# Kernel tuning notes

Hardware: AMD Instinct MI355X
Metric: run time of the kernel (lower is better)

The kernel has to match this reference:

```python
import jax, jax.numpy as jnp
import numpy as np

B, T, H, W_SP, C_IN = 8, 16, 64, 64, 32
F = 64  # output_channels


def _conv(x, w):
    # x: (B,H,W,Cin), w: (kh,kw,Cin,Cout), 'same' padding, stride 1
    return jax.lax.conv_general_dilated(
        x, w, window_strides=(1, 1), padding='SAME',
        dimension_numbers=('NHWC', 'HWIO', 'NHWC'))


def setup_inputs() -> dict:
    key = jax.random.key(0)
    k1, k2, k3 = jax.random.split(key, 3)
    x = jax.random.normal(k1, (B, T, H, W_SP, C_IN), dtype=jnp.float32)
    # Keras ConvLSTM2D kernels: gates stacked [i, f, c, o] along last axis
    W = jax.random.normal(k2, (3, 3, C_IN, 4 * F), dtype=jnp.float32) * 0.05
    U = jax.random.normal(k3, (3, 3, F, 4 * F), dtype=jnp.float32) * 0.05
    b = jnp.zeros((4 * F,), dtype=jnp.float32)
    return {"x": x, "W": W, "U": U, "b": b}


def reference(x, W, U, b):
    # ConvLSTM2D: activation='relu', recurrent_activation='hard_sigmoid',
    # return_sequences=False -> final hidden state (B,H,W,F)
    rec_act = jax.nn.hard_sigmoid  # relu6(x+3)/6
    act = jax.nn.relu

    h0 = jnp.zeros((x.shape[0], x.shape[2], x.shape[3], F), dtype=x.dtype)
    c0 = jnp.zeros_like(h0)

    def step(carry, x_t):
        h, c = carry
        z = _conv(x_t, W) + _conv(h, U) + b  # (B,H,W,4F)
        zi, zf, zc, zo = jnp.split(z, 4, axis=-1)
        i = rec_act(zi)
        f = rec_act(zf)
        o = rec_act(zo)
        c_new = f * c + i * act(zc)
        h_new = o * act(c_new)
        return (h_new, c_new), None

    xs = jnp.transpose(x, (1, 0, 2, 3, 4))  # (T,B,H,W,Cin)
    (h_final, _), _ = jax.lax.scan(step, (h0, c0), xs)
    return h_final
```

## Files before the change

### kernel.cpp

```cpp
#include <hip/hip_runtime.h>


#define TSTEPS 16

typedef short bf16x8 __attribute__((ext_vector_type(8)));
typedef float f32x4 __attribute__((ext_vector_type(4)));

__device__ __forceinline__ float hsig(float x) {
    return fminf(fmaxf((x + 3.0f) * (1.0f / 6.0f), 0.0f), 1.0f);
}

__device__ __forceinline__ unsigned short f2bf(float f) {
    union { float f; unsigned int u; } v; v.f = f;
    unsigned int r = v.u + 0x7fffu + ((v.u >> 16) & 1u);
    return (unsigned short)(r >> 16);
}

__global__ __launch_bounds__(256)
void prepack_w(const float* __restrict__ Wg, const float* __restrict__ Ug,
               unsigned short* __restrict__ out)
{
    int idx = blockIdx.x * 256 + threadIdx.x;
    if (idx >= 27648) return;
    int lane = idx & 63;
    int nt   = (idx >> 6) & 15;
    int s    = idx >> 10;
    int col = lane & 15, quad = lane >> 4;
    int n = nt * 16 + col;
    int k0 = quad * 8;
    const float* src;
    if (s < 9) {
        src = Wg + ((size_t)s * 32 + k0) * 256 + n;
    } else {
        int ss = s - 9; int tap = ss >> 1; int half = ss & 1;
        src = Ug + ((size_t)tap * 64 + half * 32 + k0) * 256 + n;
    }
    unsigned short tmp[8];
    #pragma unroll
    for (int j = 0; j < 8; ++j) tmp[j] = f2bf(src[(size_t)j * 256]);
    *(uint4*)(out + (size_t)idx * 8) = *(uint4*)tmp;
}

template<int NS>
__global__ __launch_bounds__(1024)
__attribute__((amdgpu_waves_per_eu(4, 4)))
void convlstm_step(const float* __restrict__ x,
                   const unsigned short* __restrict__ wpk,
                   const float* __restrict__ bias,
                   const unsigned short* __restrict__ h_in,
                   float* __restrict__ c_st,
                   unsigned short* __restrict__ h_out,
                   int t, int is_last)
{
    constexpr bool HP = (NS == 27);

    __shared__ __align__(16) unsigned char smem[40320];
    unsigned short* xs_s = (unsigned short*)smem;
    unsigned short* hs_s = (unsigned short*)(smem + 14400);
    float*          zbuf = (float*)smem;

    const int tid  = threadIdx.x;
    const int bid  = blockIdx.x;
    const int b    = bid & 7;
    const int tile = bid >> 3;
    const int gx0  = (tile & 7) * 8;
    const int gy0  = (tile >> 3) * 16;

    const int lane  = tid & 63;
    const int w     = tid >> 6;
    const int pxgrp = w >> 3;
    const int ngrp  = w & 7;
    const int quad  = lane >> 4;
    const int m     = lane & 15;

    uint4 hv0 = make_uint4(0u,0u,0u,0u), hv1 = make_uint4(0u,0u,0u,0u);
    int ho0 = 0, ho1 = -1;
    if constexpr (HP) {
        const unsigned short* hb = h_in + ((size_t)b * (64 * 64 * 64));
        auto issueH = [&](int idx, uint4& v, int& off) {
            int pix = idx >> 3, q = idx & 7;
            int iy = pix / 10, ix = pix - iy * 10;
            int gy = gy0 + iy - 1, gx = gx0 + ix - 1;
            if ((unsigned)gy < 64u && (unsigned)gx < 64u)
                v = *(const uint4*)(hb + ((size_t)(gy * 64 + gx) * 64) + q * 8);
            off = pix * 72 + q * 8;
        };
        issueH(tid, hv0, ho0);
        if (tid < 416) issueH(tid + 1024, hv1, ho1);
    }

    {
        const float* xt = x + (((size_t)b * TSTEPS + t) * (size_t)(64 * 64 * 32));
        #pragma unroll 2
        for (int idx = tid; idx < 180 * 8; idx += 1024) {
            int pix = idx >> 3, q = idx & 7;
            int iy = pix / 10, ix = pix - iy * 10;
            int gy = gy0 + iy - 1, gx = gx0 + ix - 1;
            unsigned short o[4] = {0, 0, 0, 0};
            if ((unsigned)gy < 64u && (unsigned)gx < 64u) {
                float4 v = *(const float4*)(xt + ((size_t)(gy * 64 + gx) * 32) + q * 4);
                o[0] = f2bf(v.x); o[1] = f2bf(v.y); o[2] = f2bf(v.z); o[3] = f2bf(v.w);
            }
            *(ushort4*)(xs_s + pix * 40 + q * 4) = *(ushort4*)o;
        }
    }
    __syncthreads();

    int xb[4], hb_[4];
    #pragma unroll
    for (int mt = 0; mt < 4; ++mt) {
        int p = mt * 16 + m;
        int row = pxgrp * 8 + (p >> 3);
        int cc  = p & 7;
        xb[mt]  = (row * 10 + cc) * 40 + quad * 8;
        hb_[mt] = (row * 10 + cc) * 72 + quad * 8;
    }

    f32x4 acc[4][2];
    #pragma unroll
    for (int g = 0; g < 2; ++g) {
        float bv = bias[(2 * ngrp + g) * 16 + m];
        f32x4 bi = (f32x4){bv, bv, bv, bv};
        #pragma unroll
        for (int mt = 0; mt < 4; ++mt) acc[mt][g] = bi;
    }

    float cpre[4][2];
    if constexpr (!HP) {
        #pragma unroll
        for (int q = 0; q < 4; ++q) { cpre[q][0] = 0.0f; cpre[q][1] = 0.0f; }
    }

    auto loadB = [&](int s, bf16x8* dst) {
        #pragma unroll
        for (int g = 0; g < 2; ++g)
            dst[g] = *(const bf16x8*)(wpk + ((size_t)(s * 16 + 2 * ngrp + g) * 64 + lane) * 8);
    };

    bf16x8 bC[2], bN[2];
    loadB(0, bC);

    #pragma unroll
    for (int s = 0; s < NS; ++s) {
        if (s + 1 < NS) loadB(s + 1, bN);

        bf16x8 a[4];
        if (s < 9) {
            int taplin = (s / 3) * 10 + (s % 3);
            #pragma unroll
            for (int mt = 0; mt < 4; ++mt)
                a[mt] = *(const bf16x8*)(xs_s + xb[mt] + taplin * 40);
        } else {
            int ss = s - 9, tap = ss >> 1, half = ss & 1;
            int taplin = (tap / 3) * 10 + (tap % 3);
            #pragma unroll
            for (int mt = 0; mt < 4; ++mt)
                a[mt] = *(const bf16x8*)(hs_s + hb_[mt] + taplin * 72 + half * 32);
        }

        #pragma unroll
        for (int g = 0; g < 2; ++g)
            #pragma unroll
            for (int mt = 0; mt < 4; ++mt)
                acc[mt][g] = __builtin_amdgcn_mfma_f32_16x16x32_bf16(a[mt], bC[g], acc[mt][g], 0, 0, 0);

        #pragma unroll
        for (int i = 0; i < 2; ++i) bC[i] = bN[i];

        if constexpr (HP) {
            if (s == 8) {
                *(uint4*)(hs_s + ho0) = hv0;
                if (ho1 >= 0) *(uint4*)(hs_s + ho1) = hv1;
                __syncthreads();
            }
            if (s == 17) {
                #pragma unroll
                for (int q = 0; q < 4; ++q)
                    #pragma unroll
                    for (int j = 0; j < 2; ++j) {
                        int cell = tid + j * 1024;
                        int pl = cell >> 6, fch = cell & 63;
                        int row = q * 4 + (pl >> 3), col = pl & 7;
                        size_t gidx = (((size_t)b * 64 + (gy0 + row)) * 64 + (gx0 + col)) * 64 + fch;
                        cpre[q][j] = c_st[gidx];
                    }
            }
        }
    }

    __syncthreads();
    #pragma unroll
    for (int q = 0; q < 4; ++q) {
        if (q) __syncthreads();
        if (pxgrp == (q >> 1)) {
            #pragma unroll
            for (int mtl = 0; mtl < 2; ++mtl) {
                int mt = 2 * (q & 1) + mtl;
                #pragma unroll
                for (int g = 0; g < 2; ++g)
                    #pragma unroll
                    for (int r = 0; r < 4; ++r) {
                        int p = mt * 16 + quad * 4 + r;
                        int rowl = (p >> 3) - (q & 1) * 4;
                        int pl = rowl * 8 + (p & 7);
                        int n = (2 * ngrp + g) * 16 + m;
                        zbuf[((pl * 64) + (n & 63)) * 4 + (n >> 6)] = acc[mt][g][r];
                    }
            }
        }
        __syncthreads();
        #pragma unroll
        for (int j = 0; j < 2; ++j) {
            int cell = tid + j * 1024;
            int pl = cell >> 6, fch = cell & 63;
            int row = q * 4 + (pl >> 3), col = pl & 7;
            float4 z = *(const float4*)(zbuf + (size_t)cell * 4);
            size_t gidx = (((size_t)b * 64 + (gy0 + row)) * 64 + (gx0 + col)) * 64 + fch;
            float cn = hsig(z.y) * cpre[q][j] + hsig(z.x) * fmaxf(z.z, 0.0f);
            float hn = hsig(z.w) * fmaxf(cn, 0.0f);
            if (is_last) {
                c_st[gidx] = hn;
            } else {
                c_st[gidx] = cn;
                h_out[gidx] = f2bf(hn);
            }
        }
    }
}

extern "C" void kernel_launch(void* const* d_in, const int* in_sizes, int n_in,
                              void* d_out, int out_size, void* d_ws, size_t ws_size,
                              hipStream_t stream) {
    const float* x  = (const float*)d_in[0];
    const float* Wg = (const float*)d_in[1];
    const float* Ug = (const float*)d_in[2];
    const float* bs = (const float*)d_in[3];

    unsigned short* wpk = (unsigned short*)d_ws;
    unsigned short* h0  = (unsigned short*)((char*)d_ws + 27 * 16 * 64 * 8 * 2);
    unsigned short* h1  = h0 + (size_t)8 * 64 * 64 * 64;
    float* cS = (float*)d_out;

    prepack_w<<<108, 256, 0, stream>>>(Wg, Ug, wpk);

    dim3 grid(256);
    dim3 block(1024);
    for (int t = 0; t < TSTEPS; ++t) {
        const unsigned short* hin = (t == 0) ? h0 : ((t & 1) ? h0 : h1);
        unsigned short* hout = (t & 1) ? h1 : h0;
        if (t == 0) {
            convlstm_step<9><<<grid, block, 0, stream>>>(x, wpk, bs, hin, cS, hout, t, 0);
        } else {
            convlstm_step<27><<<grid, block, 0, stream>>>(x, wpk, bs, hin, cS, hout,
                                                          t, (t == TSTEPS - 1) ? 1 : 0);
        }
    }
}
```

Baseline: 383.3 us.

## Remap wave N-tiling so each wave owns all four gates, drop LDS gate shuffle

Waves are reassigned so each one computes 2 pixel M-tiles across all four gates (i,f,c,o) for 16 channels, instead of 4 M-tiles by 2 gate columns. The pointwise LSTM update can then run directly from accumulator registers, which removes the zbuf LDS round trip and the four-phase barrier sequence in the epilogue. The cost is twice as many B-fragment loads per wave from global or cache. Each wave also reads half as many A fragments. The global c/h stores now follow the MFMA output layout, which may coalesce less well than the previous per-cell layout.

```diff
diff --git a/kernel.cpp b/kernel.cpp
--- a/kernel.cpp
+++ b/kernel.cpp
@@ -54,10 +54,8 @@
 {
     constexpr bool HP = (NS == 27);
 
-    __shared__ __align__(16) unsigned char smem[40320];
-    unsigned short* xs_s = (unsigned short*)smem;
-    unsigned short* hs_s = (unsigned short*)(smem + 14400);
-    float*          zbuf = (float*)smem;
+    __shared__ __align__(16) unsigned short xs_s[180 * 40];
+    __shared__ __align__(16) unsigned short hs_s[HP ? 180 * 72 : 8];
 
     const int tid  = threadIdx.x;
     const int bid  = blockIdx.x;
@@ -68,10 +66,11 @@
 
     const int lane  = tid & 63;
     const int w     = tid >> 6;
-    const int pxgrp = w >> 3;
-    const int ngrp  = w & 7;
+    const int pxgrp = w >> 2;
+    const int ngrp  = w & 3;
     const int quad  = lane >> 4;
     const int m     = lane & 15;
+    const int ch    = ngrp * 16 + m;
 
     uint4 hv0 = make_uint4(0u,0u,0u,0u), hv1 = make_uint4(0u,0u,0u,0u);
     int ho0 = 0, ho1 = -1;
@@ -106,66 +105,68 @@
     }
     __syncthreads();
 
-    int xb[4], hb_[4];
-    #pragma unroll
-    for (int mt = 0; mt < 4; ++mt) {
+    int xb[2], hb_[2];
+    #pragma unroll
+    for (int mt = 0; mt < 2; ++mt) {
         int p = mt * 16 + m;
-        int row = pxgrp * 8 + (p >> 3);
+        int row = pxgrp * 4 + (p >> 3);
         int cc  = p & 7;
         xb[mt]  = (row * 10 + cc) * 40 + quad * 8;
         hb_[mt] = (row * 10 + cc) * 72 + quad * 8;
     }
 
-    f32x4 acc[4][2];
-    #pragma unroll
-    for (int g = 0; g < 2; ++g) {
-        float bv = bias[(2 * ngrp + g) * 16 + m];
+    f32x4 acc[2][4];
+    #pragma unroll
+    for (int g = 0; g < 4; ++g) {
+        float bv = bias[g * 64 + ch];
         f32x4 bi = (f32x4){bv, bv, bv, bv};
         #pragma unroll
-        for (int mt = 0; mt < 4; ++mt) acc[mt][g] = bi;
-    }
-
-    float cpre[4][2];
+        for (int mt = 0; mt < 2; ++mt) acc[mt][g] = bi;
+    }
+
+    float cpre[2][4];
     if constexpr (!HP) {
         #pragma unroll
-        for (int q = 0; q < 4; ++q) { cpre[q][0] = 0.0f; cpre[q][1] = 0.0f; }
+        for (int mt = 0; mt < 2; ++mt)
+            #pragma unroll
+            for (int r = 0; r < 4; ++r) cpre[mt][r] = 0.0f;
     }
 
     auto loadB = [&](int s, bf16x8* dst) {
         #pragma unroll
-        for (int g = 0; g < 2; ++g)
-            dst[g] = *(const bf16x8*)(wpk + ((size_t)(s * 16 + 2 * ngrp + g) * 64 + lane) * 8);
+        for (int g = 0; g < 4; ++g)
+            dst[g] = *(const bf16x8*)(wpk + ((size_t)(s * 16 + ngrp + 4 * g) * 64 + lane) * 8);
     };
 
-    bf16x8 bC[2], bN[2];
+    bf16x8 bC[4], bN[4];
     loadB(0, bC);
 
     #pragma unroll
     for (int s = 0; s < NS; ++s) {
         if (s + 1 < NS) loadB(s + 1, bN);
 
-        bf16x8 a[4];
+        bf16x8 a[2];
         if (s < 9) {
             int taplin = (s / 3) * 10 + (s % 3);
             #pragma unroll
-            for (int mt = 0; mt < 4; ++mt)
+            for (int mt = 0; mt < 2; ++mt)
                 a[mt] = *(const bf16x8*)(xs_s + xb[mt] + taplin * 40);
         } else {
             int ss = s - 9, tap = ss >> 1, half = ss & 1;
             int taplin = (tap / 3) * 10 + (tap % 3);
             #pragma unroll
-            for (int mt = 0; mt < 4; ++mt)
+            for (int mt = 0; mt < 2; ++mt)
                 a[mt] = *(const bf16x8*)(hs_s + hb_[mt] + taplin * 72 + half * 32);
         }
 
         #pragma unroll
-        for (int g = 0; g < 2; ++g)
-            #pragma unroll
-            for (int mt = 0; mt < 4; ++mt)
+        for (int g = 0; g < 4; ++g)
+            #pragma unroll
+            for (int mt = 0; mt < 2; ++mt)
                 acc[mt][g] = __builtin_amdgcn_mfma_f32_16x16x32_bf16(a[mt], bC[g], acc[mt][g], 0, 0, 0);
 
         #pragma unroll
-        for (int i = 0; i < 2; ++i) bC[i] = bN[i];
+        for (int i = 0; i < 4; ++i) bC[i] = bN[i];
 
         if constexpr (HP) {
             if (s == 8) {
@@ -175,49 +176,31 @@
             }
             if (s == 17) {
                 #pragma unroll
-                for (int q = 0; q < 4; ++q)
-                    #pragma unroll
-                    for (int j = 0; j < 2; ++j) {
-                        int cell = tid + j * 1024;
-                        int pl = cell >> 6, fch = cell & 63;
-                        int row = q * 4 + (pl >> 3), col = pl & 7;
-                        size_t gidx = (((size_t)b * 64 + (gy0 + row)) * 64 + (gx0 + col)) * 64 + fch;
-                        cpre[q][j] = c_st[gidx];
-                    }
-            }
-        }
-    }
-
-    __syncthreads();
-    #pragma unroll
-    for (int q = 0; q < 4; ++q) {
-        if (q) __syncthreads();
-        if (pxgrp == (q >> 1)) {
-            #pragma unroll
-            for (int mtl = 0; mtl < 2; ++mtl) {
-                int mt = 2 * (q & 1) + mtl;
-                #pragma unroll
-                for (int g = 0; g < 2; ++g)
+                for (int mt = 0; mt < 2; ++mt)
                     #pragma unroll
                     for (int r = 0; r < 4; ++r) {
                         int p = mt * 16 + quad * 4 + r;
-                        int rowl = (p >> 3) - (q & 1) * 4;
-                        int pl = rowl * 8 + (p & 7);
-                        int n = (2 * ngrp + g) * 16 + m;
-                        zbuf[((pl * 64) + (n & 63)) * 4 + (n >> 6)] = acc[mt][g][r];
+                        int row = pxgrp * 4 + (p >> 3), col = p & 7;
+                        size_t gidx = (((size_t)b * 64 + (gy0 + row)) * 64 + (gx0 + col)) * 64 + ch;
+                        cpre[mt][r] = c_st[gidx];
                     }
             }
         }
-        __syncthreads();
-        #pragma unroll
-        for (int j = 0; j < 2; ++j) {
-            int cell = tid + j * 1024;
-            int pl = cell >> 6, fch = cell & 63;
-            int row = q * 4 + (pl >> 3), col = pl & 7;
-            float4 z = *(const float4*)(zbuf + (size_t)cell * 4);
-            size_t gidx = (((size_t)b * 64 + (gy0 + row)) * 64 + (gx0 + col)) * 64 + fch;
-            float cn = hsig(z.y) * cpre[q][j] + hsig(z.x) * fmaxf(z.z, 0.0f);
-            float hn = hsig(z.w) * fmaxf(cn, 0.0f);
+    }
+
+    #pragma unroll
+    for (int mt = 0; mt < 2; ++mt) {
+        #pragma unroll
+        for (int r = 0; r < 4; ++r) {
+            int p = mt * 16 + quad * 4 + r;
+            int row = pxgrp * 4 + (p >> 3), col = p & 7;
+            size_t gidx = (((size_t)b * 64 + (gy0 + row)) * 64 + (gx0 + col)) * 64 + ch;
+            float zi = acc[mt][0][r];
+            float zf = acc[mt][1][r];
+            float zc = acc[mt][2][r];
+            float zo = acc[mt][3][r];
+            float cn = hsig(zf) * cpre[mt][r] + hsig(zi) * fmaxf(zc, 0.0f);
+            float hn = hsig(zo) * fmaxf(cn, 0.0f);
             if (is_last) {
                 c_st[gidx] = hn;
             } else {
```

After: 406.0 us. 5.9% more time.
